# Kernel optimization log

Measured on AMD Instinct MI355X. Metric: run time of the kernel, lower is better.

Reference implementation:

```python
import jax, jax.numpy as jnp
import numpy as np

B, S, D = 4, 4096, 512

def setup_inputs() -> dict:
    key = jax.random.key(0)
    k1, k2, k3, k4 = jax.random.split(key, 4)
    x = jax.random.normal(k1, (B, S, D), dtype=jnp.float32)
    # torch nn.Linear weights are [out, in]; init scaled like kaiming-uniform-ish
    scale = 1.0 / np.sqrt(D)
    W_Q = jax.random.uniform(k2, (D, D), jnp.float32, -scale, scale)
    W_K = jax.random.uniform(k3, (D, D), jnp.float32, -scale, scale)
    W_V = jax.random.uniform(k4, (D, D), jnp.float32, -scale, scale)
    return {"x": x, "W_Q": W_Q, "W_K": W_K, "W_V": W_V}

def reference(x, W_Q, W_K, W_V):
    d = x.shape[-1]
    s = x.shape[1]
    # torch Linear: x @ W.T
    Q = jnp.einsum('bse,de->bsd', x, W_Q)
    K = jnp.einsum('bse,de->bsd', x, W_K)
    V = jnp.einsum('bse,de->bsd', x, W_V)
    scores = jnp.einsum('bqd,bkd->bqk', Q, K) / jnp.sqrt(jnp.float32(d))
    causal = jnp.triu(jnp.ones((s, s), dtype=bool), k=1)  # mask future positions
    scores = jnp.where(causal, -jnp.inf, scores)
    attn = jax.nn.softmax(scores, axis=-1)
    out = jnp.einsum('bqk,bkd->bqd', attn, V)
    return out
```

## Files before the change

### kernel.cpp

```cpp
#include <hip/hip_runtime.h>

typedef __attribute__((ext_vector_type(8))) __bf16 bf16x8;
typedef __attribute__((ext_vector_type(4))) float f32x4;
typedef unsigned short u16;
typedef __attribute__((ext_vector_type(4))) u16 u16x4;

#define MASKVAL -3.0e38f
#define MINIT   -1.0e38f
#define LOG2E 1.4426950408889634f

__device__ inline f32x4 zero4() { f32x4 v; v[0]=0.f; v[1]=0.f; v[2]=0.f; v[3]=0.f; return v; }

__device__ inline u16 bf16bits(float x) {
    union { __bf16 h; u16 u; } cv; cv.h = (__bf16)x; return cv.u;
}
__device__ inline float bits2f(u16 b) {
    union { unsigned u; float f; } cv; cv.u = ((unsigned)b) << 16; return cv.f;
}

__device__ inline void load_lds16(const u16* g, u16* l) {
    __builtin_amdgcn_global_load_lds((const __attribute__((address_space(1))) void*)g,
                                     (__attribute__((address_space(3))) void*)l, 16, 0, 0);
}

__global__ void convert_w(const float* __restrict__ WQ, const float* __restrict__ WK,
                          const float* __restrict__ WV, u16* __restrict__ Wb)
{
    const float qscale = 0.044194173824159216f;
    const int i8 = (blockIdx.x * 256 + threadIdx.x) * 8;
    const int seg = i8 >> 18;
    const int within = i8 & 262143;
    const float* src = (seg == 0) ? WQ : (seg == 1) ? WK : WV;
    const float sc = (seg == 0) ? qscale : 1.0f;
    f32x4 a = *(const f32x4*)(src + within);
    f32x4 b = *(const f32x4*)(src + within + 4);
    bf16x8 v;
    v[0]=(__bf16)(a[0]*sc); v[1]=(__bf16)(a[1]*sc); v[2]=(__bf16)(a[2]*sc); v[3]=(__bf16)(a[3]*sc);
    v[4]=(__bf16)(b[0]*sc); v[5]=(__bf16)(b[1]*sc); v[6]=(__bf16)(b[2]*sc); v[7]=(__bf16)(b[3]*sc);
    *(bf16x8*)(Wb + i8) = v;
}

__global__ void convert_x(const float* __restrict__ X, u16* __restrict__ Xb)
{
    const size_t i8 = ((size_t)blockIdx.x * 256 + threadIdx.x) * 8;
    f32x4 a = *(const f32x4*)(X + i8);
    f32x4 b = *(const f32x4*)(X + i8 + 4);
    bf16x8 v;
    v[0]=(__bf16)a[0]; v[1]=(__bf16)a[1]; v[2]=(__bf16)a[2]; v[3]=(__bf16)a[3];
    v[4]=(__bf16)b[0]; v[5]=(__bf16)b[1]; v[6]=(__bf16)b[2]; v[7]=(__bf16)b[3];
    *(bf16x8*)(Xb + i8) = v;
}

__global__ __launch_bounds__(256, 2)
void gemm_qkv(const u16* __restrict__ Xb, const u16* __restrict__ Wb,
              u16* __restrict__ Qb, u16* __restrict__ Kb, u16* __restrict__ Vt)
{
    __shared__ u16 As[128*32];
    __shared__ u16 Bs[128*32];
    const int t  = threadIdx.x;
    const int l  = t & 63;
    const int w  = t >> 6;
    const int c  = l & 15;
    const int qd = l >> 4;
    const int m0 = blockIdx.y * 128;
    const int nblk = blockIdx.x;
    const int n0 = nblk * 128;
    const int seg = nblk >> 2;
    const int nw0 = (nblk & 3) * 128;
    const int wm = w >> 1, wn = w & 1;
    const int lr = l >> 2;
    const int lc = (l & 3) * 8;

    f32x4 acc[4][4];
    #pragma unroll
    for (int i = 0; i < 4; i++)
        #pragma unroll
        for (int j = 0; j < 4; j++) acc[i][j] = zero4();

    for (int kk = 0; kk < 512; kk += 32) {
        #pragma unroll
        for (int i = 0; i < 2; ++i) {
            const int r0 = w*32 + i*16;
            load_lds16(&Xb[(size_t)(m0 + r0 + lr)*512 + kk + lc], &As[r0*32]);
            load_lds16(&Wb[(size_t)(n0 + r0 + lr)*512 + kk + lc], &Bs[r0*32]);
        }
        __syncthreads();
        bf16x8 af[4], bfr[4];
        #pragma unroll
        for (int mt = 0; mt < 4; mt++) af[mt]  = *(const bf16x8*)&As[(wm*64 + mt*16 + c)*32 + qd*8];
        #pragma unroll
        for (int nt = 0; nt < 4; nt++) bfr[nt] = *(const bf16x8*)&Bs[(wn*64 + nt*16 + c)*32 + qd*8];
        #pragma unroll
        for (int mt = 0; mt < 4; mt++)
            #pragma unroll
            for (int nt = 0; nt < 4; nt++)
                acc[mt][nt] = __builtin_amdgcn_mfma_f32_16x16x32_bf16(af[mt], bfr[nt], acc[mt][nt], 0, 0, 0);
        __syncthreads();
    }

    #pragma unroll
    for (int mt = 0; mt < 4; mt++) {
        #pragma unroll
        for (int nt = 0; nt < 4; nt++) {
            const int gm0 = m0 + wm*64 + mt*16 + qd*4;
            const int gn  = nw0 + wn*64 + nt*16 + c;
            if (seg == 0) {
                #pragma unroll
                for (int r = 0; r < 4; r++)
                    Qb[(size_t)(gm0 + r)*512 + gn] = bf16bits(acc[mt][nt][r]);
            } else if (seg == 1) {
                #pragma unroll
                for (int r = 0; r < 4; r++)
                    Kb[(size_t)(gm0 + r)*512 + gn] = bf16bits(acc[mt][nt][r]);
            } else {
                const int bb   = gm0 >> 12;
                const int ss   = gm0 & 4095;
                const int unit = ss >> 5;
                const int kl   = ss & 31;
                u16x4 pk;
                pk[0] = bf16bits(acc[mt][nt][0]);
                pk[1] = bf16bits(acc[mt][nt][1]);
                pk[2] = bf16bits(acc[mt][nt][2]);
                pk[3] = bf16bits(acc[mt][nt][3]);
                *(u16x4*)&Vt[((size_t)(bb*128 + unit)*512 + gn)*32 + kl] = pk;
            }
        }
    }
}

__global__ __launch_bounds__(256, 2)
void attn_chunk(const u16* __restrict__ Qb, const u16* __restrict__ Kb,
                const u16* __restrict__ Vt, u16* __restrict__ Op,
                float* __restrict__ Mp, float* __restrict__ Lp)
{
    __shared__ u16 Ks[2][32*520];
    __shared__ u16 Ps[2][64*40];
    __shared__ float Al[2][64];
    __shared__ unsigned Fl[2][4];

    const int t  = threadIdx.x;
    const int l  = t & 63;
    const int w  = t >> 6;
    const int c  = l & 15;
    const int qd = l >> 4;
    const int x  = blockIdx.x;
    const int qt = 63 - (x >> 4);
    const int j  = (x >> 2) & 3;
    const int b  = x & 3;
    const int U  = 2*qt + 2;
    const int uc = (U + 3) >> 2;
    const int it0 = j * uc;
    if (it0 >= U) return;
    const int it1 = min(U, it0 + uc) - 1;
    const int q0 = qt * 64;
    const int itSkip = 2*qt + (w >> 1);

    bf16x8 qf[16];
    {
        const size_t qrow = (size_t)(b*4096 + q0 + w*16 + c);
        #pragma unroll
        for (int ks = 0; ks < 16; ++ks)
            qf[ks] = *(const bf16x8*)&Qb[qrow*512 + ks*32 + qd*8];
    }

    f32x4 o[8][4];
    #pragma unroll
    for (int dt = 0; dt < 8; dt++)
        #pragma unroll
        for (int rt = 0; rt < 4; rt++) o[dt][rt] = zero4();
    float m_c = MINIT, l_c = 0.f;

    const u16* Kg = Kb + (size_t)(b*4096)*512;
    const u16* Vg = Vt + (size_t)(b*128)*16384;

    #pragma unroll
    for (int i = 0; i < 8; i++) {
        const int row = w*8 + i;
        load_lds16(Kg + ((size_t)(it0*32 + row))*512 + l*8, &Ks[0][row*520]);
    }

    for (int it = it0; it <= it1 + 1; ++it) {
        const int pb = (it - it0) & 1;
        __syncthreads();

        bf16x8 vf[8];
        if (it > it0) {
            const u16* vu = Vg + (size_t)(it-1)*16384 + qd*8;
            #pragma unroll
            for (int dt = 0; dt < 8; dt++)
                vf[dt] = *(const bf16x8*)(vu + (w*128 + dt*16 + c)*32);
        }
        if (it < it1) {
            #pragma unroll
            for (int i = 0; i < 8; i++) {
                const int row = w*8 + i;
                load_lds16(Kg + ((size_t)((it+1)*32 + row))*512 + l*8, &Ks[pb^1][row*520]);
            }
        }

        if (it <= it1) {
            if (it <= itSkip) {
                f32x4 s0 = zero4(), s1 = zero4();
                #pragma unroll
                for (int ks = 0; ks < 16; ++ks) {
                    bf16x8 k0 = *(const bf16x8*)&Ks[pb][c*520 + ks*32 + qd*8];
                    s0 = __builtin_amdgcn_mfma_f32_16x16x32_bf16(k0, qf[ks], s0, 0, 0, 0);
                    bf16x8 k1 = *(const bf16x8*)&Ks[pb][(16 + c)*520 + ks*32 + qd*8];
                    s1 = __builtin_amdgcn_mfma_f32_16x16x32_bf16(k1, qf[ks], s1, 0, 0, 0);
                }
                const int rowg = q0 + w*16 + c;
                if (32*it + 31 > rowg) {
                    const int k0g = 32*it + qd*4;
                    #pragma unroll
                    for (int r = 0; r < 4; r++) {
                        if (k0g + r      > rowg) s0[r] = MASKVAL;
                        if (k0g + 16 + r > rowg) s1[r] = MASKVAL;
                    }
                }
                float mloc = fmaxf(fmaxf(fmaxf(s0[0], s0[1]), fmaxf(s0[2], s0[3])),
                                   fmaxf(fmaxf(s1[0], s1[1]), fmaxf(s1[2], s1[3])));
                if (__ballot(mloc > m_c + 20.f)) {
                    float rm = mloc;
                    rm = fmaxf(rm, __shfl_xor(rm, 16));
                    rm = fmaxf(rm, __shfl_xor(rm, 32));
                    const float mnew = fmaxf(m_c, rm);
                    const float al = exp2f((m_c - mnew) * LOG2E);
                    l_c *= al;
                    m_c = mnew;
                    if (qd == 0) Al[pb][w*16 + c] = al;
                    if (l == 0) Fl[pb][w] = 1u;
                } else {
                    if (l == 0) Fl[pb][w] = 0u;
                }
                const float p0 = exp2f((s0[0] - m_c) * LOG2E);
                const float p1 = exp2f((s0[1] - m_c) * LOG2E);
                const float p2 = exp2f((s0[2] - m_c) * LOG2E);
                const float p3 = exp2f((s0[3] - m_c) * LOG2E);
                const float p4 = exp2f((s1[0] - m_c) * LOG2E);
                const float p5 = exp2f((s1[1] - m_c) * LOG2E);
                const float p6 = exp2f((s1[2] - m_c) * LOG2E);
                const float p7 = exp2f((s1[3] - m_c) * LOG2E);
                l_c += ((p0 + p1) + (p2 + p3)) + ((p4 + p5) + (p6 + p7));
                u16x4 pka, pkb;
                pka[0]=bf16bits(p0); pka[1]=bf16bits(p1); pka[2]=bf16bits(p2); pka[3]=bf16bits(p3);
                pkb[0]=bf16bits(p4); pkb[1]=bf16bits(p5); pkb[2]=bf16bits(p6); pkb[3]=bf16bits(p7);
                *(u16x4*)&Ps[pb][(w*16 + c)*40 + qd*4]      = pka;
                *(u16x4*)&Ps[pb][(w*16 + c)*40 + 16 + qd*4] = pkb;
            } else {
                u16x4 z; z[0]=0; z[1]=0; z[2]=0; z[3]=0;
                *(u16x4*)&Ps[pb][(w*16 + c)*40 + qd*4]      = z;
                *(u16x4*)&Ps[pb][(w*16 + c)*40 + 16 + qd*4] = z;
                if (l == 0) Fl[pb][w] = 0u;
            }
        }

        if (it > it0) {
            const int ppb = pb ^ 1;
            bf16x8 pfr[4];
            #pragma unroll
            for (int rt = 0; rt < 4; rt++)
                pfr[rt] = *(const bf16x8*)&Ps[ppb][(rt*16 + c)*40 + qd*8];
            #pragma unroll
            for (int rt = 0; rt < 4; rt++) {
                if (Fl[ppb][rt]) {
                    const float al = Al[ppb][rt*16 + c];
                    #pragma unroll
                    for (int dt = 0; dt < 8; dt++) {
                        o[dt][rt][0] *= al; o[dt][rt][1] *= al;
                        o[dt][rt][2] *= al; o[dt][rt][3] *= al;
                    }
                }
            }
            #pragma unroll
            for (int dt = 0; dt < 8; dt++)
                #pragma unroll
                for (int rt = 0; rt < 4; rt++)
                    o[dt][rt] = __builtin_amdgcn_mfma_f32_16x16x32_bf16(vf[dt], pfr[rt], o[dt][rt], 0, 0, 0);
        }
    }

    l_c += __shfl_xor(l_c, 16);
    l_c += __shfl_xor(l_c, 32);
    const size_t ob = ((size_t)((b*64 + qt)*4 + j))*64;
    if (qd == 0) {
        Mp[ob + w*16 + c] = m_c;
        Lp[ob + w*16 + c] = l_c;
    }
    #pragma unroll
    for (int dt = 0; dt < 8; dt++) {
        #pragma unroll
        for (int rt = 0; rt < 4; rt++) {
            u16x4 pk;
            pk[0] = bf16bits(o[dt][rt][0]); pk[1] = bf16bits(o[dt][rt][1]);
            pk[2] = bf16bits(o[dt][rt][2]); pk[3] = bf16bits(o[dt][rt][3]);
            *(u16x4*)&Op[(ob + rt*16 + c)*512 + w*128 + dt*16 + qd*4] = pk;
        }
    }
}

__global__ __launch_bounds__(256)
void combine(const u16* __restrict__ Op, const float* __restrict__ Mp,
             const float* __restrict__ Lp, float* __restrict__ out)
{
    __shared__ float sc[4][64];
    const int t  = threadIdx.x;
    const int qt = blockIdx.x;
    const int b  = blockIdx.y;
    const int U  = 2*qt + 2;
    const int uc = (U + 3) >> 2;
    const int nc = (U + uc - 1) / uc;
    const int base = (b*64 + qt)*4;

    if (t < 64) {
        float mj[4], lj[4];
        float M = MINIT;
        for (int j = 0; j < nc; j++) {
            mj[j] = Mp[(size_t)(base + j)*64 + t];
            lj[j] = Lp[(size_t)(base + j)*64 + t];
            M = fmaxf(M, mj[j]);
        }
        float denom = 0.f;
        float wj[4];
        for (int j = 0; j < nc; j++) {
            wj[j] = exp2f((mj[j] - M) * LOG2E);
            denom += wj[j] * lj[j];
        }
        const float inv = 1.0f / denom;
        for (int j = 0; j < nc; j++) sc[j][t] = wj[j] * inv;
    }
    __syncthreads();

    const int c4 = (t & 127) * 4;
    const int r0 = (t >> 7) * 32;
    for (int r = r0; r < r0 + 32; ++r) {
        float a0 = 0.f, a1 = 0.f, a2 = 0.f, a3 = 0.f;
        for (int j = 0; j < nc; j++) {
            const float s = sc[j][r];
            u16x4 v = *(const u16x4*)&Op[((size_t)(base + j)*64 + r)*512 + c4];
            a0 += s * bits2f(v[0]); a1 += s * bits2f(v[1]);
            a2 += s * bits2f(v[2]); a3 += s * bits2f(v[3]);
        }
        f32x4 res; res[0]=a0; res[1]=a1; res[2]=a2; res[3]=a3;
        *(f32x4*)&out[((size_t)(b*4096 + qt*64 + r))*512 + c4] = res;
    }
}

extern "C" void kernel_launch(void* const* d_in, const int* in_sizes, int n_in,
                              void* d_out, int out_size, void* d_ws, size_t ws_size,
                              hipStream_t stream)
{
    (void)in_sizes; (void)n_in; (void)out_size; (void)ws_size;
    const float* X  = (const float*)d_in[0];
    const float* WQ = (const float*)d_in[1];
    const float* WK = (const float*)d_in[2];
    const float* WV = (const float*)d_in[3];
    float* out = (float*)d_out;
    char* ws = (char*)d_ws;
    const size_t MB = 1024*1024;
    u16*   Qb = (u16*)(ws);
    u16*   Kb = (u16*)(ws + 16*MB);
    u16*   Vt = (u16*)(ws + 32*MB);
    u16*   Wb = (u16*)(ws + 48*MB);
    float* Mp = (float*)(ws + 50*MB);
    float* Lp = (float*)(ws + 51*MB);
    u16*   Op = (u16*)(ws + 52*MB);
    u16*   Xb = (u16*)(ws + 52*MB);

    convert_w<<<dim3(384), 256, 0, stream>>>(WQ, WK, WV, Wb);
    convert_x<<<dim3(4096), 256, 0, stream>>>(X, Xb);
    gemm_qkv<<<dim3(12, 128), 256, 0, stream>>>(Xb, Wb, Qb, Kb, Vt);
    attn_chunk<<<dim3(1024), 256, 0, stream>>>(Qb, Kb, Vt, Op, Mp, Lp);
    combine<<<dim3(64, 4), 256, 0, stream>>>(Op, Mp, Lp, out);
}
```

Measured before the change: 308.7 us.

## Split causal attention KV range into two equal chunks with balanced block pairing

Each query tile's KV range is now split into exactly two chunks of equal size (qt+1 iterations each), replacing the previous up-to-four-way split. The grid shrinks from 1024 blocks, many of which exited early, to 512 blocks. Tiles are ordered so the first half of the grid runs heavy tiles first and the second half runs light tiles, which balances load across blocks. The combine kernel is simplified to a fixed two-way merge using 8-wide vector loads. The goal is to cut idle blocks and partial-output traffic, at the cost of less parallelism for long rows. Xb is moved to its own workspace region so it no longer aliases Op.

Result: slower. 337.2 us (+9.2%).

```diff
diff --git a/kernel.cpp b/kernel.cpp
--- a/kernel.cpp
+++ b/kernel.cpp
@@ -4,6 +4,7 @@
 typedef __attribute__((ext_vector_type(4))) float f32x4;
 typedef unsigned short u16;
 typedef __attribute__((ext_vector_type(4))) u16 u16x4;
+typedef __attribute__((ext_vector_type(8))) u16 u16x8;
 
 #define MASKVAL -3.0e38f
 #define MINIT   -1.0e38f
@@ -144,14 +145,13 @@
     const int c  = l & 15;
     const int qd = l >> 4;
     const int x  = blockIdx.x;
-    const int qt = 63 - (x >> 4);
-    const int j  = (x >> 2) & 3;
-    const int b  = x & 3;
-    const int U  = 2*qt + 2;
-    const int uc = (U + 3) >> 2;
-    const int it0 = j * uc;
-    if (it0 >= U) return;
-    const int it1 = min(U, it0 + uc) - 1;
+    const int half = x >> 8;
+    const int xi = x & 255;
+    const int qt = half ? (xi >> 3) : 63 - (xi >> 3);
+    const int b  = (xi >> 1) & 3;
+    const int j  = xi & 1;
+    const int it0 = j * (qt + 1);
+    const int it1 = it0 + qt;
     const int q0 = qt * 64;
     const int itSkip = 2*qt + (w >> 1);
 
@@ -281,7 +281,7 @@
 
     l_c += __shfl_xor(l_c, 16);
     l_c += __shfl_xor(l_c, 32);
-    const size_t ob = ((size_t)((b*64 + qt)*4 + j))*64;
+    const size_t ob = ((size_t)((b*64 + qt)*2 + j))*64;
     if (qd == 0) {
         Mp[ob + w*16 + c] = m_c;
         Lp[ob + w*16 + c] = l_c;
@@ -302,46 +302,45 @@
 void combine(const u16* __restrict__ Op, const float* __restrict__ Mp,
              const float* __restrict__ Lp, float* __restrict__ out)
 {
-    __shared__ float sc[4][64];
+    __shared__ float sc[2][64];
     const int t  = threadIdx.x;
     const int qt = blockIdx.x;
     const int b  = blockIdx.y;
-    const int U  = 2*qt + 2;
-    const int uc = (U + 3) >> 2;
-    const int nc = (U + uc - 1) / uc;
-    const int base = (b*64 + qt)*4;
+    const int base = (b*64 + qt)*2;
 
     if (t < 64) {
-        float mj[4], lj[4];
-        float M = MINIT;
-        for (int j = 0; j < nc; j++) {
-            mj[j] = Mp[(size_t)(base + j)*64 + t];
-            lj[j] = Lp[(size_t)(base + j)*64 + t];
-            M = fmaxf(M, mj[j]);
-        }
-        float denom = 0.f;
-        float wj[4];
-        for (int j = 0; j < nc; j++) {
-            wj[j] = exp2f((mj[j] - M) * LOG2E);
-            denom += wj[j] * lj[j];
-        }
-        const float inv = 1.0f / denom;
-        for (int j = 0; j < nc; j++) sc[j][t] = wj[j] * inv;
+        const float m0 = Mp[(size_t)base*64 + t];
+        const float m1 = Mp[(size_t)(base + 1)*64 + t];
+        const float l0 = Lp[(size_t)base*64 + t];
+        const float l1 = Lp[(size_t)(base + 1)*64 + t];
+        const float M = fmaxf(m0, m1);
+        const float w0 = exp2f((m0 - M) * LOG2E);
+        const float w1 = exp2f((m1 - M) * LOG2E);
+        const float inv = 1.0f / (w0*l0 + w1*l1);
+        sc[0][t] = w0 * inv;
+        sc[1][t] = w1 * inv;
     }
     __syncthreads();
 
-    const int c4 = (t & 127) * 4;
-    const int r0 = (t >> 7) * 32;
-    for (int r = r0; r < r0 + 32; ++r) {
-        float a0 = 0.f, a1 = 0.f, a2 = 0.f, a3 = 0.f;
-        for (int j = 0; j < nc; j++) {
-            const float s = sc[j][r];
-            u16x4 v = *(const u16x4*)&Op[((size_t)(base + j)*64 + r)*512 + c4];
-            a0 += s * bits2f(v[0]); a1 += s * bits2f(v[1]);
-            a2 += s * bits2f(v[2]); a3 += s * bits2f(v[3]);
-        }
-        f32x4 res; res[0]=a0; res[1]=a1; res[2]=a2; res[3]=a3;
-        *(f32x4*)&out[((size_t)(b*4096 + qt*64 + r))*512 + c4] = res;
+    const int c8 = (t & 63) * 8;
+    const int r0 = (t >> 6) * 16;
+    for (int r = r0; r < r0 + 16; ++r) {
+        const float s0 = sc[0][r];
+        const float s1 = sc[1][r];
+        u16x8 v0 = *(const u16x8*)&Op[((size_t)base*64 + r)*512 + c8];
+        u16x8 v1 = *(const u16x8*)&Op[((size_t)(base + 1)*64 + r)*512 + c8];
+        f32x4 ra, rb;
+        ra[0] = s0*bits2f(v0[0]) + s1*bits2f(v1[0]);
+        ra[1] = s0*bits2f(v0[1]) + s1*bits2f(v1[1]);
+        ra[2] = s0*bits2f(v0[2]) + s1*bits2f(v1[2]);
+        ra[3] = s0*bits2f(v0[3]) + s1*bits2f(v1[3]);
+        rb[0] = s0*bits2f(v0[4]) + s1*bits2f(v1[4]);
+        rb[1] = s0*bits2f(v0[5]) + s1*bits2f(v1[5]);
+        rb[2] = s0*bits2f(v0[6]) + s1*bits2f(v1[6]);
+        rb[3] = s0*bits2f(v0[7]) + s1*bits2f(v1[7]);
+        float* op = &out[((size_t)(b*4096 + qt*64 + r))*512 + c8];
+        *(f32x4*)op       = ra;
+        *(f32x4*)(op + 4) = rb;
     }
 }
 
@@ -364,11 +363,11 @@
     float* Mp = (float*)(ws + 50*MB);
     float* Lp = (float*)(ws + 51*MB);
     u16*   Op = (u16*)(ws + 52*MB);
-    u16*   Xb = (u16*)(ws + 52*MB);
+    u16*   Xb = (u16*)(ws + 84*MB);
 
     convert_w<<<dim3(384), 256, 0, stream>>>(WQ, WK, WV, Wb);
     convert_x<<<dim3(4096), 256, 0, stream>>>(X, Xb);
     gemm_qkv<<<dim3(12, 128), 256, 0, stream>>>(Xb, Wb, Qb, Kb, Vt);
-    attn_chunk<<<dim3(1024), 256, 0, stream>>>(Qb, Kb, Vt, Op, Mp, Lp);
+    attn_chunk<<<dim3(512), 256, 0, stream>>>(Qb, Kb, Vt, Op, Mp, Lp);
     combine<<<dim3(64, 4), 256, 0, stream>>>(Op, Mp, Lp, out);
 }
```

## Interleave PV MFMAs with QK MFMAs and prefetch V one iteration ahead

Applied to the files above, without the earlier changes.

The main loop now issues the previous tile's P·V MFMAs inside the current tile's QK^T MFMA loop, alternating two QK MFMAs with four PV MFMAs. This lets matrix work overlap and fills gaps left by dependent MFMA chains. V fragments are now loaded at the end of each iteration for the next one, giving the global loads a full iteration of latency cover. The combine kernel is also widened to 8 bf16 per thread for wider loads and stores. The cost is more live registers, since vf is held across iterations, which could reduce occupancy or cause spills.

After: 837.1 us. +171.2%, slower.

```diff
diff --git a/kernel.cpp b/kernel.cpp
--- a/kernel.cpp
+++ b/kernel.cpp
@@ -4,6 +4,7 @@
 typedef __attribute__((ext_vector_type(4))) float f32x4;
 typedef unsigned short u16;
 typedef __attribute__((ext_vector_type(4))) u16 u16x4;
+typedef __attribute__((ext_vector_type(8))) u16 u16x8;
 
 #define MASKVAL -3.0e38f
 #define MINIT   -1.0e38f
@@ -169,6 +170,7 @@
         #pragma unroll
         for (int rt = 0; rt < 4; rt++) o[dt][rt] = zero4();
     float m_c = MINIT, l_c = 0.f;
+    bf16x8 vf[8];
 
     const u16* Kg = Kb + (size_t)(b*4096)*512;
     const u16* Vg = Vt + (size_t)(b*128)*16384;
@@ -183,13 +185,6 @@
         const int pb = (it - it0) & 1;
         __syncthreads();
 
-        bf16x8 vf[8];
-        if (it > it0) {
-            const u16* vu = Vg + (size_t)(it-1)*16384 + qd*8;
-            #pragma unroll
-            for (int dt = 0; dt < 8; dt++)
-                vf[dt] = *(const bf16x8*)(vu + (w*128 + dt*16 + c)*32);
-        }
         if (it < it1) {
             #pragma unroll
             for (int i = 0; i < 8; i++) {
@@ -198,65 +193,10 @@
             }
         }
 
-        if (it <= it1) {
-            if (it <= itSkip) {
-                f32x4 s0 = zero4(), s1 = zero4();
-                #pragma unroll
-                for (int ks = 0; ks < 16; ++ks) {
-                    bf16x8 k0 = *(const bf16x8*)&Ks[pb][c*520 + ks*32 + qd*8];
-                    s0 = __builtin_amdgcn_mfma_f32_16x16x32_bf16(k0, qf[ks], s0, 0, 0, 0);
-                    bf16x8 k1 = *(const bf16x8*)&Ks[pb][(16 + c)*520 + ks*32 + qd*8];
-                    s1 = __builtin_amdgcn_mfma_f32_16x16x32_bf16(k1, qf[ks], s1, 0, 0, 0);
-                }
-                const int rowg = q0 + w*16 + c;
-                if (32*it + 31 > rowg) {
-                    const int k0g = 32*it + qd*4;
-                    #pragma unroll
-                    for (int r = 0; r < 4; r++) {
-                        if (k0g + r      > rowg) s0[r] = MASKVAL;
-                        if (k0g + 16 + r > rowg) s1[r] = MASKVAL;
-                    }
-                }
-                float mloc = fmaxf(fmaxf(fmaxf(s0[0], s0[1]), fmaxf(s0[2], s0[3])),
-                                   fmaxf(fmaxf(s1[0], s1[1]), fmaxf(s1[2], s1[3])));
-                if (__ballot(mloc > m_c + 20.f)) {
-                    float rm = mloc;
-                    rm = fmaxf(rm, __shfl_xor(rm, 16));
-                    rm = fmaxf(rm, __shfl_xor(rm, 32));
-                    const float mnew = fmaxf(m_c, rm);
-                    const float al = exp2f((m_c - mnew) * LOG2E);
-                    l_c *= al;
-                    m_c = mnew;
-                    if (qd == 0) Al[pb][w*16 + c] = al;
-                    if (l == 0) Fl[pb][w] = 1u;
-                } else {
-                    if (l == 0) Fl[pb][w] = 0u;
-                }
-                const float p0 = exp2f((s0[0] - m_c) * LOG2E);
-                const float p1 = exp2f((s0[1] - m_c) * LOG2E);
-                const float p2 = exp2f((s0[2] - m_c) * LOG2E);
-                const float p3 = exp2f((s0[3] - m_c) * LOG2E);
-                const float p4 = exp2f((s1[0] - m_c) * LOG2E);
-                const float p5 = exp2f((s1[1] - m_c) * LOG2E);
-                const float p6 = exp2f((s1[2] - m_c) * LOG2E);
-                const float p7 = exp2f((s1[3] - m_c) * LOG2E);
-                l_c += ((p0 + p1) + (p2 + p3)) + ((p4 + p5) + (p6 + p7));
-                u16x4 pka, pkb;
-                pka[0]=bf16bits(p0); pka[1]=bf16bits(p1); pka[2]=bf16bits(p2); pka[3]=bf16bits(p3);
-                pkb[0]=bf16bits(p4); pkb[1]=bf16bits(p5); pkb[2]=bf16bits(p6); pkb[3]=bf16bits(p7);
-                *(u16x4*)&Ps[pb][(w*16 + c)*40 + qd*4]      = pka;
-                *(u16x4*)&Ps[pb][(w*16 + c)*40 + 16 + qd*4] = pkb;
-            } else {
-                u16x4 z; z[0]=0; z[1]=0; z[2]=0; z[3]=0;
-                *(u16x4*)&Ps[pb][(w*16 + c)*40 + qd*4]      = z;
-                *(u16x4*)&Ps[pb][(w*16 + c)*40 + 16 + qd*4] = z;
-                if (l == 0) Fl[pb][w] = 0u;
-            }
-        }
-
-        if (it > it0) {
+        const bool haveP = (it > it0);
+        bf16x8 pfr[4];
+        if (haveP) {
             const int ppb = pb ^ 1;
-            bf16x8 pfr[4];
             #pragma unroll
             for (int rt = 0; rt < 4; rt++)
                 pfr[rt] = *(const bf16x8*)&Ps[ppb][(rt*16 + c)*40 + qd*8];
@@ -271,11 +211,93 @@
                     }
                 }
             }
+        }
+
+        if (it <= it1 && it <= itSkip) {
+            f32x4 s0 = zero4(), s1 = zero4();
+            if (haveP) {
+                #pragma unroll
+                for (int ks = 0; ks < 16; ++ks) {
+                    bf16x8 k0 = *(const bf16x8*)&Ks[pb][c*520 + ks*32 + qd*8];
+                    s0 = __builtin_amdgcn_mfma_f32_16x16x32_bf16(k0, qf[ks], s0, 0, 0, 0);
+                    bf16x8 k1 = *(const bf16x8*)&Ks[pb][(16 + c)*520 + ks*32 + qd*8];
+                    s1 = __builtin_amdgcn_mfma_f32_16x16x32_bf16(k1, qf[ks], s1, 0, 0, 0);
+                    if (ks & 1) {
+                        const int dt = ks >> 1;
+                        #pragma unroll
+                        for (int rt = 0; rt < 4; rt++)
+                            o[dt][rt] = __builtin_amdgcn_mfma_f32_16x16x32_bf16(vf[dt], pfr[rt], o[dt][rt], 0, 0, 0);
+                    }
+                }
+            } else {
+                #pragma unroll
+                for (int ks = 0; ks < 16; ++ks) {
+                    bf16x8 k0 = *(const bf16x8*)&Ks[pb][c*520 + ks*32 + qd*8];
+                    s0 = __builtin_amdgcn_mfma_f32_16x16x32_bf16(k0, qf[ks], s0, 0, 0, 0);
+                    bf16x8 k1 = *(const bf16x8*)&Ks[pb][(16 + c)*520 + ks*32 + qd*8];
+                    s1 = __builtin_amdgcn_mfma_f32_16x16x32_bf16(k1, qf[ks], s1, 0, 0, 0);
+                }
+            }
+
+            const int rowg = q0 + w*16 + c;
+            if (32*it + 31 > rowg) {
+                const int k0g = 32*it + qd*4;
+                #pragma unroll
+                for (int r = 0; r < 4; r++) {
+                    if (k0g + r      > rowg) s0[r] = MASKVAL;
+                    if (k0g + 16 + r > rowg) s1[r] = MASKVAL;
+                }
+            }
+            float mloc = fmaxf(fmaxf(fmaxf(s0[0], s0[1]), fmaxf(s0[2], s0[3])),
+                               fmaxf(fmaxf(s1[0], s1[1]), fmaxf(s1[2], s1[3])));
+            if (__ballot(mloc > m_c + 20.f)) {
+                float rm = mloc;
+                rm = fmaxf(rm, __shfl_xor(rm, 16));
+                rm = fmaxf(rm, __shfl_xor(rm, 32));
+                const float mnew = fmaxf(m_c, rm);
+                const float al = exp2f((m_c - mnew) * LOG2E);
+                l_c *= al;
+                m_c = mnew;
+                if (qd == 0) Al[pb][w*16 + c] = al;
+                if (l == 0) Fl[pb][w] = 1u;
+            } else {
+                if (l == 0) Fl[pb][w] = 0u;
+            }
+            const float p0 = exp2f((s0[0] - m_c) * LOG2E);
+            const float p1 = exp2f((s0[1] - m_c) * LOG2E);
+            const float p2 = exp2f((s0[2] - m_c) * LOG2E);
+            const float p3 = exp2f((s0[3] - m_c) * LOG2E);
+            const float p4 = exp2f((s1[0] - m_c) * LOG2E);
+            const float p5 = exp2f((s1[1] - m_c) * LOG2E);
+            const float p6 = exp2f((s1[2] - m_c) * LOG2E);
+            const float p7 = exp2f((s1[3] - m_c) * LOG2E);
+            l_c += ((p0 + p1) + (p2 + p3)) + ((p4 + p5) + (p6 + p7));
+            u16x4 pka, pkb;
+            pka[0]=bf16bits(p0); pka[1]=bf16bits(p1); pka[2]=bf16bits(p2); pka[3]=bf16bits(p3);
+            pkb[0]=bf16bits(p4); pkb[1]=bf16bits(p5); pkb[2]=bf16bits(p6); pkb[3]=bf16bits(p7);
+            *(u16x4*)&Ps[pb][(w*16 + c)*40 + qd*4]      = pka;
+            *(u16x4*)&Ps[pb][(w*16 + c)*40 + 16 + qd*4] = pkb;
+        } else {
+            if (haveP) {
+                #pragma unroll
+                for (int dt = 0; dt < 8; dt++)
+                    #pragma unroll
+                    for (int rt = 0; rt < 4; rt++)
+                        o[dt][rt] = __builtin_amdgcn_mfma_f32_16x16x32_bf16(vf[dt], pfr[rt], o[dt][rt], 0, 0, 0);
+            }
+            if (it <= it1) {
+                u16x4 z; z[0]=0; z[1]=0; z[2]=0; z[3]=0;
+                *(u16x4*)&Ps[pb][(w*16 + c)*40 + qd*4]      = z;
+                *(u16x4*)&Ps[pb][(w*16 + c)*40 + 16 + qd*4] = z;
+                if (l == 0) Fl[pb][w] = 0u;
+            }
+        }
+
+        if (it <= it1) {
+            const u16* vu = Vg + (size_t)it*16384 + qd*8;
             #pragma unroll
             for (int dt = 0; dt < 8; dt++)
-                #pragma unroll
-                for (int rt = 0; rt < 4; rt++)
-                    o[dt][rt] = __builtin_amdgcn_mfma_f32_16x16x32_bf16(vf[dt], pfr[rt], o[dt][rt], 0, 0, 0);
+                vf[dt] = *(const bf16x8*)(vu + (w*128 + dt*16 + c)*32);
         }
     }
 
@@ -330,18 +352,24 @@
     }
     __syncthreads();
 
-    const int c4 = (t & 127) * 4;
-    const int r0 = (t >> 7) * 32;
-    for (int r = r0; r < r0 + 32; ++r) {
-        float a0 = 0.f, a1 = 0.f, a2 = 0.f, a3 = 0.f;
+    const int c8 = (t & 63) * 8;
+    const int r0 = (t >> 6) * 16;
+    for (int r = r0; r < r0 + 16; ++r) {
+        float a0=0.f, a1=0.f, a2=0.f, a3=0.f, a4=0.f, a5=0.f, a6=0.f, a7=0.f;
         for (int j = 0; j < nc; j++) {
             const float s = sc[j][r];
-            u16x4 v = *(const u16x4*)&Op[((size_t)(base + j)*64 + r)*512 + c4];
-            a0 += s * bits2f(v[0]); a1 += s * bits2f(v[1]);
-            a2 += s * bits2f(v[2]); a3 += s * bits2f(v[3]);
-        }
-        f32x4 res; res[0]=a0; res[1]=a1; res[2]=a2; res[3]=a3;
-        *(f32x4*)&out[((size_t)(b*4096 + qt*64 + r))*512 + c4] = res;
+            u16x8 v = *(const u16x8*)&Op[((size_t)(base + j)*64 + r)*512 + c8];
+            a0 += s*bits2f(v[0]); a1 += s*bits2f(v[1]);
+            a2 += s*bits2f(v[2]); a3 += s*bits2f(v[3]);
+            a4 += s*bits2f(v[4]); a5 += s*bits2f(v[5]);
+            a6 += s*bits2f(v[6]); a7 += s*bits2f(v[7]);
+        }
+        f32x4 ra, rb;
+        ra[0]=a0; ra[1]=a1; ra[2]=a2; ra[3]=a3;
+        rb[0]=a4; rb[1]=a5; rb[2]=a6; rb[3]=a7;
+        float* op = &out[((size_t)(b*4096 + qt*64 + r))*512 + c8];
+        *(f32x4*)op       = ra;
+        *(f32x4*)(op + 4) = rb;
     }
 }
 
```
